# Kernel tuning notes

Measured on AMD Instinct MI355X. Metric: run time of the kernel, lower is better.

Reference implementation:

```python
import jax, jax.numpy as jnp
import numpy as np

N_NODES = 50000
N_EDGES = 1600000
X_DIM = 128
HID = 128
HEADS = 8
C1 = HID // HEADS  # 16 per-head channels in gnn1
N_GRAPHS = 500
SLOPE = 0.3       # negative_slope (alpha in source)
BN_EPS = 1e-5


def segment_softmax(e, idx, n):
    # numerically stable softmax over segments defined by idx
    m = jax.ops.segment_max(e, idx, num_segments=n)
    ex = jnp.exp(e - m[idx])
    s = jax.ops.segment_sum(ex, idx, num_segments=n)
    return ex / (s[idx] + 1e-16)


def gatv2(x, src, dst, Wl, Wr, att, bias, heads, ch, concat):
    # PyG GATv2Conv (share_weights=False, edge_dim=None), eval mode (no dropout)
    n = x.shape[0]
    xl = (x @ Wl).reshape(n, heads, ch)  # messages (source side)
    xr = (x @ Wr).reshape(n, heads, ch)  # target side
    h = jax.nn.leaky_relu(xl[src] + xr[dst], SLOPE)      # [E,H,C]
    score = jnp.einsum('ehc,hc->eh', h, att)             # [E,H]
    alpha = segment_softmax(score, dst, n)               # softmax over in-edges of each target
    out = jax.ops.segment_sum(xl[src] * alpha[:, :, None], dst, num_segments=n)  # [N,H,C]
    out = out.reshape(n, heads * ch) if concat else out.mean(axis=1)
    return out + bias


def batchnorm_eval(x, g, b, rm, rv):
    return (x - rm) * (g / jnp.sqrt(rv + BN_EPS)) + b


def setup_inputs() -> dict:
    key = jax.random.key(0)
    ks = jax.random.split(key, 16)
    s = 0.05
    return {
        'x': jax.random.normal(ks[0], (N_NODES, X_DIM), jnp.float32),
        'edge_index': jax.random.randint(ks[1], (2, N_EDGES), 0, N_NODES, jnp.int32),
        'batch': jnp.sort(jax.random.randint(ks[2], (N_NODES,), 0, N_GRAPHS, jnp.int32)),
        # gnn1: GATv2Conv(x_dim -> hid//8, heads=8, concat)
        'Wl1': jax.random.normal(ks[3], (X_DIM, HID), jnp.float32) * s,
        'Wr1': jax.random.normal(ks[4], (X_DIM, HID), jnp.float32) * s,
        'att1': jax.random.normal(ks[5], (HEADS, C1), jnp.float32) * s,
        'b1': jnp.zeros((HID,), jnp.float32),
        # gnn2: GATv2Conv(hid -> hid, heads=1, concat=False)
        'Wl2': jax.random.normal(ks[6], (HID, HID), jnp.float32) * s,
        'Wr2': jax.random.normal(ks[7], (HID, HID), jnp.float32) * s,
        'att2': jax.random.normal(ks[8], (1, HID), jnp.float32) * s,
        'b2': jnp.zeros((HID,), jnp.float32),
        # shared BatchNorm1d(hid), eval mode buffers + affine
        'bn_g': jnp.ones((HID,), jnp.float32),
        'bn_b': jnp.zeros((HID,), jnp.float32),
        'bn_rm': jnp.zeros((HID,), jnp.float32),
        'bn_rv': jnp.ones((HID,), jnp.float32),
        # attentional aggregation gate_nn: Linear->Tanh->Linear(no bias)
        'Wg1': jax.random.normal(ks[9], (HID, HID), jnp.float32) * s,
        'bg1': jnp.zeros((HID,), jnp.float32),
        'Wg2': jax.random.normal(ks[10], (HID, 1), jnp.float32) * s,
        # fc_out: Linear(hid,100)->ReLU->Linear(100,1)
        'Wf1': jax.random.normal(ks[11], (HID, 100), jnp.float32) * s,
        'bf1': jnp.zeros((100,), jnp.float32),
        'Wf2': jax.random.normal(ks[12], (100, 1), jnp.float32) * s,
        'bf2': jnp.zeros((1,), jnp.float32),
    }


def reference(x, edge_index, batch, Wl1, Wr1, att1, b1, Wl2, Wr2, att2, b2,
              bn_g, bn_b, bn_rm, bn_rv, Wg1, bg1, Wg2, Wf1, bf1, Wf2, bf2):
    src, dst = edge_index[0], edge_index[1]
    # GAT layer 1 (8 heads, concat) -> dropout(eval no-op) -> BN -> ReLU
    h1 = gatv2(x, src, dst, Wl1, Wr1, att1, b1, HEADS, C1, True)
    h1 = jax.nn.relu(batchnorm_eval(h1, bn_g, bn_b, bn_rm, bn_rv))
    # GAT layer 2 (1 head, mean/no-concat) -> BN -> ReLU
    h2 = gatv2(h1, src, dst, Wl2, Wr2, att2, b2, 1, HID, False)
    h2 = jax.nn.relu(batchnorm_eval(h2, bn_g, bn_b, bn_rm, bn_rv))
    # AttentionalAggregation: softmax(gate_nn(x), batch) weighted sum
    gate = jnp.tanh(h2 @ Wg1 + bg1) @ Wg2                 # [N,1]
    gate = segment_softmax(gate, batch, N_GRAPHS)
    pooled = jax.ops.segment_sum(gate * h2, batch, num_segments=N_GRAPHS)  # [B,HID]
    # fc_out head
    return jax.nn.relu(pooled @ Wf1 + bf1) @ Wf2 + bf2    # [B,1]
```

## Files before the change

kernel.cpp:

```cpp
#include <hip/hip_runtime.h>
#include <hip/hip_fp16.h>
#include <math.h>

#define NEG_SLOPE 0.3f
#define BN_EPS 1e-5f
#define DEG_CAP 96

static __device__ __forceinline__ int lower_bound_i(const int* __restrict__ a, int n, int v) {
  int lo = 0, hi = n;
  while (lo < hi) {
    int mid = (lo + hi) >> 1;
    if (a[mid] < v) lo = mid + 1; else hi = mid;
  }
  return lo;
}

__global__ __launch_bounds__(256) void gemm2_kernel(const float* __restrict__ A,
    const float* __restrict__ W1, const float* __restrict__ W2,
    __half* __restrict__ C1h, float* __restrict__ C2, int n,
    const int* __restrict__ src, const int* __restrict__ dst, int ne,
    int* __restrict__ cursor, int* __restrict__ csr_src,
    const float* __restrict__ b1, const float* __restrict__ b2,
    const float* __restrict__ g, const float* __restrict__ bb,
    const float* __restrict__ rm, const float* __restrict__ rv,
    float* __restrict__ s1, float* __restrict__ h1s,
    float* __restrict__ s2, float* __restrict__ h2s,
    int gemm_blocks, int total_gs) {
  __shared__ float As[64 * 128];
  if (blockIdx.x >= total_gs) {
    int t = threadIdx.x;
    int c = t & 127;
    float s = g[c] / sqrtf(rv[c] + BN_EPS);
    const float* bias = (t < 128) ? b1 : b2;
    float* so = (t < 128) ? s1 : s2;
    float* ho = (t < 128) ? h1s : h2s;
    so[c] = s;
    ho[c] = (bias[c] - rm[c]) * s + bb[c];
    return;
  }
  if (blockIdx.x >= gemm_blocks) {
    int tid = (blockIdx.x - gemm_blocks) * 256 + threadIdx.x;
    int stride = (total_gs - gemm_blocks) * 256;
    int nb4 = ne >> 2;
    const int4* s4p = (const int4*)src;
    const int4* d4p = (const int4*)dst;
    for (int i = tid; i < nb4; i += stride) {
      int4 s4 = s4p[i];
      int4 d4 = d4p[i];
      csr_src[d4.x * DEG_CAP + atomicAdd(&cursor[d4.x], 1)] = s4.x;
      csr_src[d4.y * DEG_CAP + atomicAdd(&cursor[d4.y], 1)] = s4.y;
      csr_src[d4.z * DEG_CAP + atomicAdd(&cursor[d4.z], 1)] = s4.z;
      csr_src[d4.w * DEG_CAP + atomicAdd(&cursor[d4.w], 1)] = s4.w;
    }
    for (int i = (nb4 << 2) + tid; i < ne; i += stride) {
      int d = dst[i];
      csr_src[d * DEG_CAP + atomicAdd(&cursor[d], 1)] = src[i];
    }
    return;
  }
  int t = threadIdx.x;
  int r0 = blockIdx.x << 6;
  {
    float4* Asv = (float4*)As;
    if (r0 + 64 <= n) {
      const float4* Av = (const float4*)(A + (size_t)r0 * 128);
#pragma unroll
      for (int i = 0; i < 8; ++i) Asv[t + 256 * i] = Av[t + 256 * i];
    } else {
#pragma unroll
      for (int i = 0; i < 8; ++i) {
        int idx = t + 256 * i;
        int rr = idx >> 5;
        int cc = idx & 31;
        int gr = min(r0 + rr, n - 1);
        Asv[idx] = ((const float4*)(A + (size_t)gr * 128))[cc];
      }
    }
  }
  __syncthreads();
  int cg = t & 31;
  int rg = t >> 5;
  const float4* W1v = (const float4*)W1;
  const float4* W2v = (const float4*)W2;
  float4 a1[8], a2[8];
#pragma unroll
  for (int r = 0; r < 8; ++r) {
    a1[r] = make_float4(0.f, 0.f, 0.f, 0.f);
    a2[r] = make_float4(0.f, 0.f, 0.f, 0.f);
  }
  float4 u0 = W1v[0 * 32 + cg], u1 = W1v[1 * 32 + cg];
  float4 u2 = W1v[2 * 32 + cg], u3 = W1v[3 * 32 + cg];
  float4 v0 = W2v[0 * 32 + cg], v1 = W2v[1 * 32 + cg];
  float4 v2 = W2v[2 * 32 + cg], v3 = W2v[3 * 32 + cg];
#pragma unroll 2
  for (int kg = 0; kg < 32; ++kg) {
    int k = kg << 2;
    int kn = (kg < 31) ? (k + 4) : 0;
    float4 nu0 = W1v[(kn + 0) * 32 + cg];
    float4 nu1 = W1v[(kn + 1) * 32 + cg];
    float4 nu2 = W1v[(kn + 2) * 32 + cg];
    float4 nu3 = W1v[(kn + 3) * 32 + cg];
    float4 nv0 = W2v[(kn + 0) * 32 + cg];
    float4 nv1 = W2v[(kn + 1) * 32 + cg];
    float4 nv2 = W2v[(kn + 2) * 32 + cg];
    float4 nv3 = W2v[(kn + 3) * 32 + cg];
#pragma unroll
    for (int r = 0; r < 8; ++r) {
      float4 av = *(const float4*)&As[(rg * 8 + r) * 128 + k];
      a1[r].x += av.x * u0.x + av.y * u1.x + av.z * u2.x + av.w * u3.x;
      a1[r].y += av.x * u0.y + av.y * u1.y + av.z * u2.y + av.w * u3.y;
      a1[r].z += av.x * u0.z + av.y * u1.z + av.z * u2.z + av.w * u3.z;
      a1[r].w += av.x * u0.w + av.y * u1.w + av.z * u2.w + av.w * u3.w;
      a2[r].x += av.x * v0.x + av.y * v1.x + av.z * v2.x + av.w * v3.x;
      a2[r].y += av.x * v0.y + av.y * v1.y + av.z * v2.y + av.w * v3.y;
      a2[r].z += av.x * v0.z + av.y * v1.z + av.z * v2.z + av.w * v3.z;
      a2[r].w += av.x * v0.w + av.y * v1.w + av.z * v2.w + av.w * v3.w;
    }
    u0 = nu0; u1 = nu1; u2 = nu2; u3 = nu3;
    v0 = nv0; v1 = nv1; v2 = nv2; v3 = nv3;
  }
#pragma unroll
  for (int r = 0; r < 8; ++r) {
    int gr = r0 + rg * 8 + r;
    if (gr < n) {
      __half2 hx = __floats2half2_rn(a1[r].x, a1[r].y);
      __half2 hy = __floats2half2_rn(a1[r].z, a1[r].w);
      uint2 pk;
      pk.x = *(unsigned int*)&hx;
      pk.y = *(unsigned int*)&hy;
      ((uint2*)C1h)[(size_t)gr * 32 + cg] = pk;
      *(float4*)&C2[(size_t)gr * 128 + cg * 4] = a2[r];
    }
  }
}

__global__ __launch_bounds__(256) void gate_kernel(const float* __restrict__ A,
    const float* __restrict__ Wg1, const float* __restrict__ bg1,
    const float* __restrict__ Wg2, float* __restrict__ gate, int n) {
  __shared__ float As[64 * 128];
  int t = threadIdx.x;
  int r0 = blockIdx.x << 6;
  {
    float4* Asv = (float4*)As;
    if (r0 + 64 <= n) {
      const float4* Av = (const float4*)(A + (size_t)r0 * 128);
#pragma unroll
      for (int i = 0; i < 8; ++i) Asv[t + 256 * i] = Av[t + 256 * i];
    } else {
#pragma unroll
      for (int i = 0; i < 8; ++i) {
        int idx = t + 256 * i;
        int rr = idx >> 5;
        int cc = idx & 31;
        int gr = min(r0 + rr, n - 1);
        Asv[idx] = ((const float4*)(A + (size_t)gr * 128))[cc];
      }
    }
  }
  __syncthreads();
  int cg = t & 31;
  int rg = t >> 5;
  const float4* Wv = (const float4*)Wg1;
  float4 bg4 = *(const float4*)&bg1[cg * 4];
  float4 wg4 = *(const float4*)&Wg2[cg * 4];
  float4 acc[8];
#pragma unroll
  for (int r = 0; r < 8; ++r) acc[r] = make_float4(0.f, 0.f, 0.f, 0.f);
  float4 w0 = Wv[0 * 32 + cg];
  float4 w1 = Wv[1 * 32 + cg];
  float4 w2 = Wv[2 * 32 + cg];
  float4 w3 = Wv[3 * 32 + cg];
#pragma unroll 4
  for (int kg = 0; kg < 32; ++kg) {
    int k = kg << 2;
    int kn = (kg < 31) ? (k + 4) : 0;
    float4 nw0 = Wv[(kn + 0) * 32 + cg];
    float4 nw1 = Wv[(kn + 1) * 32 + cg];
    float4 nw2 = Wv[(kn + 2) * 32 + cg];
    float4 nw3 = Wv[(kn + 3) * 32 + cg];
#pragma unroll
    for (int r = 0; r < 8; ++r) {
      float4 av = *(const float4*)&As[(rg * 8 + r) * 128 + k];
      acc[r].x += av.x * w0.x + av.y * w1.x + av.z * w2.x + av.w * w3.x;
      acc[r].y += av.x * w0.y + av.y * w1.y + av.z * w2.y + av.w * w3.y;
      acc[r].z += av.x * w0.z + av.y * w1.z + av.z * w2.z + av.w * w3.z;
      acc[r].w += av.x * w0.w + av.y * w1.w + av.z * w2.w + av.w * w3.w;
    }
    w0 = nw0; w1 = nw1; w2 = nw2; w3 = nw3;
  }
#pragma unroll
  for (int r = 0; r < 8; ++r) {
    float v = tanhf(acc[r].x + bg4.x) * wg4.x
            + tanhf(acc[r].y + bg4.y) * wg4.y
            + tanhf(acc[r].z + bg4.z) * wg4.z
            + tanhf(acc[r].w + bg4.w) * wg4.w;
    v += __shfl_xor(v, 1);
    v += __shfl_xor(v, 2);
    v += __shfl_xor(v, 4);
    v += __shfl_xor(v, 8);
    v += __shfl_xor(v, 16);
    int gr = r0 + rg * 8 + r;
    if (cg == 0 && gr < n) gate[gr] = v;
  }
}

template<bool REDUCE>
__global__ __launch_bounds__(64) void gat_fused(
    const __half* __restrict__ xlh, const float* __restrict__ xr,
    const int* __restrict__ csr_src, const int* __restrict__ deg,
    const float* __restrict__ att,
    const float* __restrict__ bnscale, const float* __restrict__ bnshift,
    float* __restrict__ out, int n_nodes) {
  int n = blockIdx.x;
  if (n >= n_nodes) return;
  int l = threadIdx.x;
  int c = l & 7;
  int es = l >> 3;

  float at8[2][8], xr8[2][8];
  {
    const float4* atp = (const float4*)att;
    const float4* xrp = (const float4*)(xr + (size_t)n * 128);
#pragma unroll
    for (int j = 0; j < 2; ++j) {
#pragma unroll
      for (int q = 0; q < 2; ++q) {
        float4 a = atp[2 * c + 16 * j + q];
        float4 xv = xrp[2 * c + 16 * j + q];
        at8[j][4 * q + 0] = a.x; at8[j][4 * q + 1] = a.y;
        at8[j][4 * q + 2] = a.z; at8[j][4 * q + 3] = a.w;
        xr8[j][4 * q + 0] = xv.x; xr8[j][4 * q + 1] = xv.y;
        xr8[j][4 * q + 2] = xv.z; xr8[j][4 * q + 3] = xv.w;
      }
    }
  }
  int d = deg[n];
  float acc[16];
#pragma unroll
  for (int j = 0; j < 16; ++j) acc[j] = 0.f;
  float ssum[2] = {0.f, 0.f};

  const int* cp = csr_src + (size_t)n * DEG_CAP;
  int iters = (d + 7) >> 3;

  auto loadgrp = [&](int eidx, float4* raw) -> bool {
    bool valid = eidx < d;
    int ecl = valid ? eidx : (d - 1);
    int sidx = cp[ecl];
    const float4* xp = (const float4*)(xlh + (size_t)sidx * 128);
    raw[0] = xp[c];
    raw[1] = xp[c + 8];
    return valid;
  };
  auto compute = [&](const float4* raw, bool valid) {
    float v[16];
#pragma unroll
    for (int j = 0; j < 2; ++j) {
      const __half2* hp = (const __half2*)&raw[j];
#pragma unroll
      for (int q = 0; q < 4; ++q) {
        float2 f = __half22float2(hp[q]);
        v[8 * j + 2 * q + 0] = f.x;
        v[8 * j + 2 * q + 1] = f.y;
      }
    }
    float p[2];
#pragma unroll
    for (int j = 0; j < 2; ++j) {
      float pj = 0.f;
#pragma unroll
      for (int k = 0; k < 8; ++k) {
        float t = v[8 * j + k] + xr8[j][k];
        pj += at8[j][k] * (fmaxf(t, 0.f) + NEG_SLOPE * fminf(t, 0.f));
      }
      p[j] = pj;
    }
    if (REDUCE) {
      float q = p[0] + p[1];
      q += __shfl_xor(q, 1);
      q += __shfl_xor(q, 2);
      q += __shfl_xor(q, 4);
      float ex = valid ? __expf(q) : 0.f;
      ssum[0] += ex;
#pragma unroll
      for (int k = 0; k < 16; ++k) acc[k] += ex * v[k];
    } else {
#pragma unroll
      for (int j = 0; j < 2; ++j) {
        p[j] += __shfl_xor(p[j], 1);
        float ex = valid ? __expf(p[j]) : 0.f;
        ssum[j] += ex;
#pragma unroll
        for (int k = 0; k < 8; ++k) acc[8 * j + k] += ex * v[8 * j + k];
      }
    }
  };

  int i = 0;
  for (; i + 2 <= iters; i += 2) {
    float4 r0[2], r1[2];
    bool a = loadgrp((i << 3) + es, r0);
    bool b = loadgrp(((i + 1) << 3) + es, r1);
    compute(r0, a);
    compute(r1, b);
  }
  if (i < iters) {
    float4 r0[2];
    bool a = loadgrp((i << 3) + es, r0);
    compute(r0, a);
  }

#pragma unroll
  for (int st = 8; st <= 32; st <<= 1) {
    if (REDUCE) {
      ssum[0] += __shfl_xor(ssum[0], st);
    } else {
      ssum[0] += __shfl_xor(ssum[0], st);
      ssum[1] += __shfl_xor(ssum[1], st);
    }
#pragma unroll
    for (int j = 0; j < 16; ++j) acc[j] += __shfl_xor(acc[j], st);
  }

  if (es == 0) {
    float inv[2];
    if (REDUCE) {
      float iv = 1.f / (ssum[0] + 1e-16f);
      inv[0] = iv; inv[1] = iv;
    } else {
      inv[0] = 1.f / (ssum[0] + 1e-16f);
      inv[1] = 1.f / (ssum[1] + 1e-16f);
    }
    const float4* scp = (const float4*)bnscale;
    const float4* shp = (const float4*)bnshift;
    float4* op = (float4*)(out + (size_t)n * 128);
#pragma unroll
    for (int j = 0; j < 2; ++j) {
#pragma unroll
      for (int q = 0; q < 2; ++q) {
        int slot = 2 * c + 16 * j + q;
        float4 sc = scp[slot], sh = shp[slot];
        float4 o;
        o.x = fmaxf(acc[8 * j + 4 * q + 0] * inv[j] * sc.x + sh.x, 0.f);
        o.y = fmaxf(acc[8 * j + 4 * q + 1] * inv[j] * sc.y + sh.y, 0.f);
        o.z = fmaxf(acc[8 * j + 4 * q + 2] * inv[j] * sc.z + sh.z, 0.f);
        o.w = fmaxf(acc[8 * j + 4 * q + 3] * inv[j] * sc.w + sh.w, 0.f);
        op[slot] = o;
      }
    }
  }
}

__global__ __launch_bounds__(128) void poolfc_kernel(const float* __restrict__ gate,
    const float* __restrict__ h2, const int* __restrict__ batch, int n_nodes,
    const float* __restrict__ Wf1, const float* __restrict__ bf1,
    const float* __restrict__ Wf2, const float* __restrict__ bf2,
    float* __restrict__ out, int n_graphs) {
  int g = blockIdx.x;
  if (g >= n_graphs) return;
  int t = threadIdx.x;
  int start = lower_bound_i(batch, n_nodes, g);
  int end = lower_bound_i(batch, n_nodes, g + 1);
  __shared__ float red[128];
  __shared__ float pl[128];
  float m = -__builtin_inff();
  for (int i = start + t; i < end; i += 128) m = fmaxf(m, gate[i]);
  red[t] = m;
  __syncthreads();
  for (int off = 64; off >= 1; off >>= 1) {
    if (t < off) red[t] = fmaxf(red[t], red[t + off]);
    __syncthreads();
  }
  m = red[0];
  __syncthreads();
  float s = 0.f, acc = 0.f;
  for (int i = start; i < end; ++i) {
    float ex = __expf(gate[i] - m);
    s += ex;
    acc += ex * h2[(size_t)i * 128 + t];
  }
  pl[t] = acc / (s + 1e-16f);
  __syncthreads();
  float v = 0.f;
  if (t < 100) {
    float a = bf1[t];
    for (int k = 0; k < 128; ++k) a += pl[k] * Wf1[k * 100 + t];
    v = fmaxf(a, 0.f) * Wf2[t];
  }
  red[t] = v;
  __syncthreads();
  for (int off = 64; off >= 1; off >>= 1) {
    if (t < off) red[t] += red[t + off];
    __syncthreads();
  }
  if (t == 0) out[g] = red[0] + bf2[0];
}

extern "C" void kernel_launch(void* const* d_in, const int* in_sizes, int n_in,
                              void* d_out, int out_size, void* d_ws, size_t ws_size,
                              hipStream_t stream) {
  const float* x     = (const float*)d_in[0];
  const int*   ei    = (const int*)d_in[1];
  const int*   batch = (const int*)d_in[2];
  const float* Wl1   = (const float*)d_in[3];
  const float* Wr1   = (const float*)d_in[4];
  const float* att1  = (const float*)d_in[5];
  const float* b1    = (const float*)d_in[6];
  const float* Wl2   = (const float*)d_in[7];
  const float* Wr2   = (const float*)d_in[8];
  const float* att2  = (const float*)d_in[9];
  const float* b2    = (const float*)d_in[10];
  const float* bn_g  = (const float*)d_in[11];
  const float* bn_b  = (const float*)d_in[12];
  const float* bn_rm = (const float*)d_in[13];
  const float* bn_rv = (const float*)d_in[14];
  const float* Wg1   = (const float*)d_in[15];
  const float* bg1   = (const float*)d_in[16];
  const float* Wg2   = (const float*)d_in[17];
  const float* Wf1   = (const float*)d_in[18];
  const float* bf1   = (const float*)d_in[19];
  const float* Wf2   = (const float*)d_in[20];
  const float* bf2   = (const float*)d_in[21];

  const int N  = in_sizes[0] / 128;
  const int E  = in_sizes[1] / 2;
  const int NG = out_size;
  const int* src = ei;
  const int* dst = ei + E;

  char* p = (char*)d_ws;
  auto alloc = [&](size_t bytes) -> void* {
    void* r = (void*)p;
    p += (bytes + 255) & ~(size_t)255;
    return r;
  };
  __half* xlh    = (__half*)alloc((size_t)N * 128 * 2);
  float* bufB    = (float*)alloc((size_t)N * 128 * 4);
  float* h1      = (float*)alloc((size_t)N * 128 * 4);
  int*   cursor  = (int*)alloc((size_t)N * 4);
  int*   csr_src = (int*)alloc((size_t)N * DEG_CAP * 4);
  float* gate    = (float*)alloc((size_t)N * 4);
  float* bns1    = (float*)alloc(128 * 4);
  float* bnh1    = (float*)alloc(128 * 4);
  float* bns2    = (float*)alloc(128 * 4);
  float* bnh2    = (float*)alloc(128 * 4);
  float* h2      = h1;

  const int gemm_blocks = (N + 63) >> 6;
  const int scat_blocks = 1024;
  const int total_gs = gemm_blocks + scat_blocks;

  hipMemsetAsync(cursor, 0, (size_t)N * 4, stream);
  gemm2_kernel<<<total_gs + 1, 256, 0, stream>>>(
      x, Wl1, Wr1, xlh, bufB, N, src, dst, E, cursor, csr_src,
      b1, b2, bn_g, bn_b, bn_rm, bn_rv, bns1, bnh1, bns2, bnh2,
      gemm_blocks, total_gs);
  gat_fused<false><<<N, 64, 0, stream>>>(xlh, bufB, csr_src, cursor, att1,
                                         bns1, bnh1, h1, N);
  gemm2_kernel<<<gemm_blocks, 256, 0, stream>>>(
      h1, Wl2, Wr2, xlh, bufB, N, nullptr, nullptr, 0, nullptr, nullptr,
      nullptr, nullptr, nullptr, nullptr, nullptr, nullptr,
      nullptr, nullptr, nullptr, nullptr, gemm_blocks, gemm_blocks);
  gat_fused<true><<<N, 64, 0, stream>>>(xlh, bufB, csr_src, cursor, att2,
                                        bns2, bnh2, h2, N);
  gate_kernel<<<gemm_blocks, 256, 0, stream>>>(h2, Wg1, bg1, Wg2, gate, N);
  poolfc_kernel<<<NG, 128, 0, stream>>>(gate, h2, batch, N, Wf1, bf1, Wf2, bf2,
                                        (float*)d_out, NG);
}
```

Baseline: 476.9 us.

## Co-schedule edge scatter inside GEMM blocks using extra warps and nontemporal stores

Instead of giving the CSR edge scatter its own 1024 blocks, each GEMM block is widened to 512 threads. The upper 256 threads perform the atomic scatter while the lower 256 threads run the dense projection. CSR writes now use nontemporal stores so they pollute the cache less. The goal is to overlap the latency-bound atomic scatter with GEMM compute inside the same workgroups, at the cost of larger blocks and a 512-thread launch bound that may constrain register allocation. The second layer still launches with 256 threads, so the t>=256 scatter path is skipped there.

```diff
diff --git a/kernel.cpp b/kernel.cpp
--- a/kernel.cpp
+++ b/kernel.cpp
@@ -15,7 +15,7 @@
   return lo;
 }
 
-__global__ __launch_bounds__(256) void gemm2_kernel(const float* __restrict__ A,
+__global__ __launch_bounds__(512) void gemm2_kernel(const float* __restrict__ A,
     const float* __restrict__ W1, const float* __restrict__ W2,
     __half* __restrict__ C1h, float* __restrict__ C2, int n,
     const int* __restrict__ src, const int* __restrict__ dst, int ne,
@@ -25,42 +25,24 @@
     const float* __restrict__ rm, const float* __restrict__ rv,
     float* __restrict__ s1, float* __restrict__ h1s,
     float* __restrict__ s2, float* __restrict__ h2s,
-    int gemm_blocks, int total_gs) {
+    int gemm_blocks) {
   __shared__ float As[64 * 128];
-  if (blockIdx.x >= total_gs) {
+  if (blockIdx.x >= (unsigned)gemm_blocks) {
     int t = threadIdx.x;
-    int c = t & 127;
-    float s = g[c] / sqrtf(rv[c] + BN_EPS);
-    const float* bias = (t < 128) ? b1 : b2;
-    float* so = (t < 128) ? s1 : s2;
-    float* ho = (t < 128) ? h1s : h2s;
-    so[c] = s;
-    ho[c] = (bias[c] - rm[c]) * s + bb[c];
-    return;
-  }
-  if (blockIdx.x >= gemm_blocks) {
-    int tid = (blockIdx.x - gemm_blocks) * 256 + threadIdx.x;
-    int stride = (total_gs - gemm_blocks) * 256;
-    int nb4 = ne >> 2;
-    const int4* s4p = (const int4*)src;
-    const int4* d4p = (const int4*)dst;
-    for (int i = tid; i < nb4; i += stride) {
-      int4 s4 = s4p[i];
-      int4 d4 = d4p[i];
-      csr_src[d4.x * DEG_CAP + atomicAdd(&cursor[d4.x], 1)] = s4.x;
-      csr_src[d4.y * DEG_CAP + atomicAdd(&cursor[d4.y], 1)] = s4.y;
-      csr_src[d4.z * DEG_CAP + atomicAdd(&cursor[d4.z], 1)] = s4.z;
-      csr_src[d4.w * DEG_CAP + atomicAdd(&cursor[d4.w], 1)] = s4.w;
-    }
-    for (int i = (nb4 << 2) + tid; i < ne; i += stride) {
-      int d = dst[i];
-      csr_src[d * DEG_CAP + atomicAdd(&cursor[d], 1)] = src[i];
+    if (t < 256) {
+      int c = t & 127;
+      float s = g[c] / sqrtf(rv[c] + BN_EPS);
+      const float* bias = (t < 128) ? b1 : b2;
+      float* so = (t < 128) ? s1 : s2;
+      float* ho = (t < 128) ? h1s : h2s;
+      so[c] = s;
+      ho[c] = (bias[c] - rm[c]) * s + bb[c];
     }
     return;
   }
   int t = threadIdx.x;
   int r0 = blockIdx.x << 6;
-  {
+  if (t < 256) {
     float4* Asv = (float4*)As;
     if (r0 + 64 <= n) {
       const float4* Av = (const float4*)(A + (size_t)r0 * 128);
@@ -78,6 +60,28 @@
     }
   }
   __syncthreads();
+  if (t >= 256) {
+    if (ne > 0) {
+      int tid = blockIdx.x * 256 + (t - 256);
+      int stride = gemm_blocks * 256;
+      int nb4 = ne >> 2;
+      const int4* s4p = (const int4*)src;
+      const int4* d4p = (const int4*)dst;
+      for (int i = tid; i < nb4; i += stride) {
+        int4 s4 = s4p[i];
+        int4 d4 = d4p[i];
+        __builtin_nontemporal_store(s4.x, &csr_src[d4.x * DEG_CAP + atomicAdd(&cursor[d4.x], 1)]);
+        __builtin_nontemporal_store(s4.y, &csr_src[d4.y * DEG_CAP + atomicAdd(&cursor[d4.y], 1)]);
+        __builtin_nontemporal_store(s4.z, &csr_src[d4.z * DEG_CAP + atomicAdd(&cursor[d4.z], 1)]);
+        __builtin_nontemporal_store(s4.w, &csr_src[d4.w * DEG_CAP + atomicAdd(&cursor[d4.w], 1)]);
+      }
+      for (int i = (nb4 << 2) + tid; i < ne; i += stride) {
+        int d = dst[i];
+        __builtin_nontemporal_store(src[i], &csr_src[d * DEG_CAP + atomicAdd(&cursor[d], 1)]);
+      }
+    }
+    return;
+  }
   int cg = t & 31;
   int rg = t >> 5;
   const float4* W1v = (const float4*)W1;
@@ -447,20 +451,18 @@
   float* h2      = h1;
 
   const int gemm_blocks = (N + 63) >> 6;
-  const int scat_blocks = 1024;
-  const int total_gs = gemm_blocks + scat_blocks;
 
   hipMemsetAsync(cursor, 0, (size_t)N * 4, stream);
-  gemm2_kernel<<<total_gs + 1, 256, 0, stream>>>(
+  gemm2_kernel<<<gemm_blocks + 1, 512, 0, stream>>>(
       x, Wl1, Wr1, xlh, bufB, N, src, dst, E, cursor, csr_src,
       b1, b2, bn_g, bn_b, bn_rm, bn_rv, bns1, bnh1, bns2, bnh2,
-      gemm_blocks, total_gs);
+      gemm_blocks);
   gat_fused<false><<<N, 64, 0, stream>>>(xlh, bufB, csr_src, cursor, att1,
                                          bns1, bnh1, h1, N);
   gemm2_kernel<<<gemm_blocks, 256, 0, stream>>>(
       h1, Wl2, Wr2, xlh, bufB, N, nullptr, nullptr, 0, nullptr, nullptr,
       nullptr, nullptr, nullptr, nullptr, nullptr, nullptr,
-      nullptr, nullptr, nullptr, nullptr, gemm_blocks, gemm_blocks);
+      nullptr, nullptr, nullptr, nullptr, gemm_blocks);
   gat_fused<true><<<N, 64, 0, stream>>>(xlh, bufB, csr_src, cursor, att2,
                                         bns2, bnh2, h2, N);
   gate_kernel<<<gemm_blocks, 256, 0, stream>>>(h2, Wg1, bg1, Wg2, gate, N);
```

After: 525.3 us. 10.1% more time.
